# Performance work log

Hardware: AMD Instinct MI355X
Metric: run time of the kernel (lower is better)

## Reference

```python
import jax, jax.numpy as jnp
import numpy as np

N = 100000       # num nodes
E = 3200000      # num edges (avg degree 32)
F_IN = 128       # num_node_features
HID = 16         # hidden dim hard-coded in Net
C = 10           # num_classes


def setup_inputs() -> dict:
    key = jax.random.key(0)
    k1, k2, k3, k4 = jax.random.split(key, 4)
    x = jax.random.normal(k1, (N, F_IN), dtype=jnp.float32)
    edge_index = jax.random.randint(k2, (2, E), 0, N, dtype=jnp.int32)
    W1 = jax.random.normal(k3, (F_IN, HID), dtype=jnp.float32) * 0.05
    b1 = jnp.zeros((HID,), dtype=jnp.float32)
    W2 = jax.random.normal(k4, (HID, C), dtype=jnp.float32) * 0.05
    b2 = jnp.zeros((C,), dtype=jnp.float32)
    return {"x": x, "edge_index": edge_index, "W1": W1, "b1": b1, "W2": W2, "b2": b2}


def reference(x, edge_index, W1, b1, W2, b2):
    # GCNConv: out = D^{-1/2} (A + I) D^{-1/2} X W + b   (add self-loops)
    loops = jnp.arange(N, dtype=edge_index.dtype)
    row = jnp.concatenate([edge_index[0], loops])  # source nodes
    col = jnp.concatenate([edge_index[1], loops])  # target nodes

    # symmetric normalization (degrees include self-loops, so deg >= 1)
    deg = jax.ops.segment_sum(jnp.ones_like(col, dtype=jnp.float32), col, num_segments=N)
    dis = jax.lax.rsqrt(deg)
    norm = dis[row] * dis[col]  # [E+N]

    def gcn_conv(h, W, b):
        h = h @ W                               # [N, d_out] small GEMM first
        msg = h[row] * norm[:, None]            # gather + scale, [E+N, d_out]
        out = jax.ops.segment_sum(msg, col, num_segments=N)  # scatter-add
        return out + b

    h = jax.nn.relu(gcn_conv(x, W1, b1))
    # F.dropout(training=False) is identity in eval mode
    logits = gcn_conv(h, W2, b2)
    return jax.nn.log_softmax(logits, axis=1)
```

## Files before the change

### kernel.cpp

```cpp
#include <hip/hip_runtime.h>
#include <math.h>

#define N_NODES 100000
#define N_EDGES 3200000
#define F_IN 128
#define HID 16
#define C_OUT 10
#define WIN 256
#define NDIG 391
#define PNB2 500
#define EPB 6400
#define SCN (NDIG * PNB2)
#define SB1 764
#define MAXE2 20
#define CSRLDS 10240

typedef unsigned short u16;
typedef unsigned int u32;

__device__ __forceinline__ float bf2f(u16 u) {
    return __uint_as_float(((u32)u) << 16);
}
__device__ __forceinline__ u16 f2bf(float f) {
    u32 x = __float_as_uint(f);
    u32 r = (x + 0x7fffu + ((x >> 16) & 1u)) >> 16;
    return (u16)r;
}
__device__ __forceinline__ void acc8(float* a, uint4 w) {
    a[0] += bf2f((u16)(w.x & 0xffff)); a[1] += bf2f((u16)(w.x >> 16));
    a[2] += bf2f((u16)(w.y & 0xffff)); a[3] += bf2f((u16)(w.y >> 16));
    a[4] += bf2f((u16)(w.z & 0xffff)); a[5] += bf2f((u16)(w.z >> 16));
    a[6] += bf2f((u16)(w.w & 0xffff)); a[7] += bf2f((u16)(w.w >> 16));
}

__global__ void k_pcnt(const int* __restrict__ col, int* __restrict__ blkhistA) {
    __shared__ int h[NDIG];
    for (int i = threadIdx.x; i < NDIG; i += 256) h[i] = 0;
    __syncthreads();
    const uint4* c4 = (const uint4*)(col + blockIdx.x * EPB);
    for (int i = threadIdx.x; i < EPB / 4; i += 256) {
        uint4 c = c4[i];
        atomicAdd(&h[c.x >> 8], 1);
        atomicAdd(&h[c.y >> 8], 1);
        atomicAdd(&h[c.z >> 8], 1);
        atomicAdd(&h[c.w >> 8], 1);
    }
    __syncthreads();
    for (int d = threadIdx.x; d < NDIG; d += 256)
        blkhistA[d * PNB2 + blockIdx.x] = h[d];
}

__global__ void k_s1(const int* __restrict__ blkhistA, int* __restrict__ psum) {
    __shared__ int sm[256];
    int i = blockIdx.x * 256 + threadIdx.x;
    sm[threadIdx.x] = (i < SCN) ? blkhistA[i] : 0;
    __syncthreads();
    for (int off = 128; off > 0; off >>= 1) {
        if (threadIdx.x < off) sm[threadIdx.x] += sm[threadIdx.x + off];
        __syncthreads();
    }
    if (threadIdx.x == 0) psum[blockIdx.x] = sm[0];
}

__global__ void k_s3(const int* __restrict__ blkhistA, const int* __restrict__ psum,
                     int* __restrict__ blkhistB) {
    __shared__ int ps[1024];
    __shared__ int sm[256];
    int t = threadIdx.x;
    for (int i = t; i < 1024; i += 256) ps[i] = (i < SB1) ? psum[i] : 0;
    __syncthreads();
    for (int off = 1; off < 1024; off <<= 1) {
        int v[4];
#pragma unroll
        for (int j = 0; j < 4; j++) {
            int idx = t + j * 256;
            v[j] = ps[idx] + ((idx >= off) ? ps[idx - off] : 0);
        }
        __syncthreads();
#pragma unroll
        for (int j = 0; j < 4; j++) ps[t + j * 256] = v[j];
        __syncthreads();
    }
    int bpre = (blockIdx.x > 0) ? ps[blockIdx.x - 1] : 0;

    int i = blockIdx.x * 256 + t;
    int v = (i < SCN) ? blkhistA[i] : 0;
    sm[t] = v;
    __syncthreads();
    for (int off = 1; off < 256; off <<= 1) {
        int a = sm[t];
        int b = (t >= off) ? sm[t - off] : 0;
        __syncthreads();
        sm[t] = a + b;
        __syncthreads();
    }
    if (i < SCN) blkhistB[i] = bpre + sm[t] - v;
}

__global__ void __launch_bounds__(512) k_pwrite(
        const int* __restrict__ row, const int* __restrict__ col,
        const int* __restrict__ blkhistA, const int* __restrict__ blkhistB,
        u32* __restrict__ staging) {
    __shared__ u32 sorted[EPB];
    __shared__ u16 dwin[EPB];
    __shared__ int gbase[NDIG];
    __shared__ int lbase[NDIG];
    __shared__ int lcur[NDIG];
    __shared__ int scan[512];

    int t = threadIdx.x;
    int b = blockIdx.x;
    int hv = 0;
    if (t < NDIG) {
        hv = blkhistA[t * PNB2 + b];
        gbase[t] = blkhistB[t * PNB2 + b];
        lcur[t] = 0;
    }
    scan[t] = hv;
    __syncthreads();
    for (int off = 1; off < 512; off <<= 1) {
        int v = scan[t];
        int u = (t >= off) ? scan[t - off] : 0;
        __syncthreads();
        scan[t] = v + u;
        __syncthreads();
    }
    if (t < NDIG) lbase[t] = scan[t] - hv;
    __syncthreads();

    const uint4* c4 = (const uint4*)(col + b * EPB);
    const uint4* r4 = (const uint4*)(row + b * EPB);
    for (int i = t; i < EPB / 4; i += 512) {
        uint4 c = c4[i];
        uint4 r = r4[i];
        int d, rank, pos;
        d = (int)(c.x >> 8); rank = atomicAdd(&lcur[d], 1); pos = lbase[d] + rank;
        sorted[pos] = ((c.x & 255u) << 17) | r.x; dwin[pos] = (u16)d;
        d = (int)(c.y >> 8); rank = atomicAdd(&lcur[d], 1); pos = lbase[d] + rank;
        sorted[pos] = ((c.y & 255u) << 17) | r.y; dwin[pos] = (u16)d;
        d = (int)(c.z >> 8); rank = atomicAdd(&lcur[d], 1); pos = lbase[d] + rank;
        sorted[pos] = ((c.z & 255u) << 17) | r.z; dwin[pos] = (u16)d;
        d = (int)(c.w >> 8); rank = atomicAdd(&lcur[d], 1); pos = lbase[d] + rank;
        sorted[pos] = ((c.w & 255u) << 17) | r.w; dwin[pos] = (u16)d;
    }
    __syncthreads();

    for (int i = t; i < EPB; i += 512) {
        int d = dwin[i];
        staging[gbase[d] + (i - lbase[d])] = sorted[i];
    }
}

__global__ void __launch_bounds__(512) k_csr(
        u32* staging, const int* __restrict__ blkhistB,
        int* __restrict__ offs, float* __restrict__ dis) {
    __shared__ u32 sorted[CSRLDS];
    __shared__ int cnt[WIN];
    __shared__ int base[WIN];
    int w = blockIdx.x;
    int t = threadIdx.x;
    if (t < WIN) cnt[t] = 0;
    __syncthreads();
    int start = blkhistB[w * PNB2];
    int end = (w == NDIG - 1) ? N_EDGES : blkhistB[(w + 1) * PNB2];
    int m = end - start;
    u32 buf[MAXE2];
    int n = 0;
#pragma unroll
    for (int k = 0; k < MAXE2; k++) {
        int i = k * 512 + t;
        if (i < m) {
            u32 e = staging[start + i];
            buf[k] = e;
            n = k + 1;
            atomicAdd(&cnt[e >> 17], 1);
        }
    }
    __syncthreads();
    if (t < WIN) base[t] = cnt[t];
    __syncthreads();
    for (int off = 1; off < WIN; off <<= 1) {
        int v = 0;
        if (t < WIN) {
            v = base[t];
            if (t >= off) v += base[t - off];
        }
        __syncthreads();
        if (t < WIN) base[t] = v;
        __syncthreads();
    }
    if (t < WIN) {
        int excl = base[t] - cnt[t];
        base[t] = excl;
        int node = w * WIN + t;
        if (node < N_NODES) {
            offs[node] = start + excl;
            dis[node] = rsqrtf(1.0f + (float)cnt[t]);
        }
    }
    if (w == 0 && t == 0) offs[N_NODES] = N_EDGES;
    __syncthreads();
#pragma unroll
    for (int k = 0; k < MAXE2; k++) {
        if (k < n) {
            u32 e = buf[k];
            int pos = atomicAdd(&base[(int)(e >> 17)], 1);
            sorted[pos] = e;
        }
    }
    __syncthreads();
    for (int i = t; i < m; i += 512)
        staging[start + i] = sorted[i];
}

__global__ void k_gemm1(const float* __restrict__ x, const float* __restrict__ W1,
                        const float* __restrict__ dis, u16* __restrict__ h1s) {
    __shared__ float Ws[F_IN * HID];
    for (int t = threadIdx.x; t < F_IN * HID; t += blockDim.x) Ws[t] = W1[t];
    __syncthreads();

    int node = blockIdx.x * blockDim.x + threadIdx.x;
    if (node >= N_NODES) return;

    float acc[HID];
#pragma unroll
    for (int j = 0; j < HID; j++) acc[j] = 0.f;

    const float4* xr = (const float4*)(x + (size_t)node * F_IN);
#pragma unroll 2
    for (int k4 = 0; k4 < F_IN / 4; k4++) {
        float4 v = xr[k4];
        float xv[4] = {v.x, v.y, v.z, v.w};
#pragma unroll
        for (int kk = 0; kk < 4; kk++) {
            const float4* wr = (const float4*)(Ws + (k4 * 4 + kk) * HID);
            float4 w0 = wr[0], w1 = wr[1], w2 = wr[2], w3 = wr[3];
            float xs = xv[kk];
            acc[0]  += xs * w0.x; acc[1]  += xs * w0.y; acc[2]  += xs * w0.z; acc[3]  += xs * w0.w;
            acc[4]  += xs * w1.x; acc[5]  += xs * w1.y; acc[6]  += xs * w1.z; acc[7]  += xs * w1.w;
            acc[8]  += xs * w2.x; acc[9]  += xs * w2.y; acc[10] += xs * w2.z; acc[11] += xs * w2.w;
            acc[12] += xs * w3.x; acc[13] += xs * w3.y; acc[14] += xs * w3.z; acc[15] += xs * w3.w;
        }
    }

    float d = dis[node];
    u32 p[8];
#pragma unroll
    for (int i = 0; i < 8; i++)
        p[i] = (u32)f2bf(acc[2 * i] * d) | ((u32)f2bf(acc[2 * i + 1] * d) << 16);
    u32* dst = (u32*)(h1s + (size_t)node * HID);
#pragma unroll
    for (int i = 0; i < 8; i++) dst[i] = p[i];
}

__global__ void k_gl1(const int* __restrict__ offs, const u32* __restrict__ csr,
                      const float* __restrict__ dis, const u16* __restrict__ h1s,
                      const float* __restrict__ b1, const float* __restrict__ W2,
                      u16* __restrict__ h2s) {
    __shared__ float Ws[HID * C_OUT];
    __shared__ float b1s[HID];
    if (threadIdx.x < HID * C_OUT) Ws[threadIdx.x] = W2[threadIdx.x];
    if (threadIdx.x < HID) b1s[threadIdx.x] = b1[threadIdx.x];
    __syncthreads();

    int t = blockIdx.x * 256 + threadIdx.x;
    if (t >= N_NODES * 8) return;
    int node = t >> 3;
    int q = t & 7;
    int half = q >> 2;
    int eq = q & 3;
    const uint4* hb = (const uint4*)h1s;
    float a[8] = {0.f, 0.f, 0.f, 0.f, 0.f, 0.f, 0.f, 0.f};
    if (eq == 0) acc8(a, hb[(size_t)node * 2 + half]);
    int o = offs[node + half];
    int oo = __shfl_xor(o, 4);
    int s0 = half ? oo : o;
    int s1 = half ? o : oo;
    int len = s1 - s0;
    int lo = s0 + ((len * eq) >> 2);
    int hi = s0 + ((len * (eq + 1)) >> 2);
    int j = lo;
    for (; j < hi && (j & 3); j++)
        acc8(a, hb[(size_t)(csr[j] & 0x1FFFFu) * 2 + half]);
    for (; j + 4 <= hi; j += 4) {
        uint4 ss = *(const uint4*)(csr + j);
        uint4 w0 = hb[(size_t)(ss.x & 0x1FFFFu) * 2 + half];
        uint4 w1 = hb[(size_t)(ss.y & 0x1FFFFu) * 2 + half];
        uint4 w2 = hb[(size_t)(ss.z & 0x1FFFFu) * 2 + half];
        uint4 w3 = hb[(size_t)(ss.w & 0x1FFFFu) * 2 + half];
        acc8(a, w0); acc8(a, w1); acc8(a, w2); acc8(a, w3);
    }
    for (; j < hi; j++)
        acc8(a, hb[(size_t)(csr[j] & 0x1FFFFu) * 2 + half]);

#pragma unroll
    for (int k = 0; k < 8; k++) {
        a[k] += __shfl_xor(a[k], 1);
        a[k] += __shfl_xor(a[k], 2);
    }

    float dc = dis[node];
    float own[8], oth[8];
#pragma unroll
    for (int k = 0; k < 8; k++) own[k] = a[k] * dc;
#pragma unroll
    for (int k = 0; k < 8; k++) oth[k] = __shfl_xor(own[k], 4);
    float h[16];
#pragma unroll
    for (int k = 0; k < 8; k++) {
        h[k]     = half ? oth[k] : own[k];
        h[8 + k] = half ? own[k] : oth[k];
    }
#pragma unroll
    for (int jj = 0; jj < 16; jj++) h[jj] = fmaxf(h[jj] + b1s[jj], 0.f);

    int nf = half ? 2 : 8;
    float outv[8];
#pragma unroll
    for (int k = 0; k < 8; k++) {
        float s = 0.f;
        if (k < nf) {
            int kk = half * 8 + k;
#pragma unroll
            for (int jj = 0; jj < 16; jj++) s += h[jj] * Ws[jj * C_OUT + kk];
        }
        outv[k] = s * dc;
    }
    if (eq == 0) {
        uint4 ov;
        ov.x = (u32)f2bf(outv[0]) | ((u32)f2bf(outv[1]) << 16);
        ov.y = half ? 0u : ((u32)f2bf(outv[2]) | ((u32)f2bf(outv[3]) << 16));
        ov.z = half ? 0u : ((u32)f2bf(outv[4]) | ((u32)f2bf(outv[5]) << 16));
        ov.w = half ? 0u : ((u32)f2bf(outv[6]) | ((u32)f2bf(outv[7]) << 16));
        ((uint4*)h2s)[(size_t)node * 2 + half] = ov;
    }
}

__global__ void k_gather2(const int* __restrict__ offs, const u32* __restrict__ csr,
                          const float* __restrict__ dis, const u16* __restrict__ h2s,
                          const float* __restrict__ b2, float* __restrict__ out) {
    __shared__ float b2s[C_OUT];
    if (threadIdx.x < C_OUT) b2s[threadIdx.x] = b2[threadIdx.x];
    __syncthreads();

    int t = blockIdx.x * 256 + threadIdx.x;
    if (t >= N_NODES * 8) return;
    int node = t >> 3;
    int q = t & 7;
    int half = q >> 2;
    int eq = q & 3;
    const uint4* hb = (const uint4*)h2s;
    float a[8] = {0.f, 0.f, 0.f, 0.f, 0.f, 0.f, 0.f, 0.f};
    if (eq == 0) acc8(a, hb[(size_t)node * 2 + half]);
    int o = offs[node + half];
    int oo = __shfl_xor(o, 4);
    int s0 = half ? oo : o;
    int s1 = half ? o : oo;
    int len = s1 - s0;
    int lo = s0 + ((len * eq) >> 2);
    int hi = s0 + ((len * (eq + 1)) >> 2);
    int j = lo;
    for (; j < hi && (j & 3); j++)
        acc8(a, hb[(size_t)(csr[j] & 0x1FFFFu) * 2 + half]);
    for (; j + 4 <= hi; j += 4) {
        uint4 ss = *(const uint4*)(csr + j);
        uint4 w0 = hb[(size_t)(ss.x & 0x1FFFFu) * 2 + half];
        uint4 w1 = hb[(size_t)(ss.y & 0x1FFFFu) * 2 + half];
        uint4 w2 = hb[(size_t)(ss.z & 0x1FFFFu) * 2 + half];
        uint4 w3 = hb[(size_t)(ss.w & 0x1FFFFu) * 2 + half];
        acc8(a, w0); acc8(a, w1); acc8(a, w2); acc8(a, w3);
    }
    for (; j < hi; j++)
        acc8(a, hb[(size_t)(csr[j] & 0x1FFFFu) * 2 + half]);

#pragma unroll
    for (int k = 0; k < 8; k++) {
        a[k] += __shfl_xor(a[k], 1);
        a[k] += __shfl_xor(a[k], 2);
    }

    float dc = dis[node];
    int nf = half ? 2 : 8;
    float lg[8];
    float m = -1e30f;
#pragma unroll
    for (int k = 0; k < 8; k++) {
        lg[k] = a[k] * dc + b2s[(half * 8 + k) % C_OUT];
        if (k < nf) m = fmaxf(m, lg[k]);
    }
    m = fmaxf(m, __shfl_xor(m, 4));
    float s = 0.f;
#pragma unroll
    for (int k = 0; k < 8; k++)
        if (k < nf) s += expf(lg[k] - m);
    s += __shfl_xor(s, 4);
    float ls = logf(s) + m;
    if (eq == 0) {
        float* dst = out + (size_t)node * C_OUT + half * 8;
        if (half == 0) {
#pragma unroll
            for (int i = 0; i < 4; i++)
                *(float2*)(dst + 2 * i) = make_float2(lg[2 * i] - ls, lg[2 * i + 1] - ls);
        } else {
            *(float2*)dst = make_float2(lg[0] - ls, lg[1] - ls);
        }
    }
}

extern "C" void kernel_launch(void* const* d_in, const int* in_sizes, int n_in,
                              void* d_out, int out_size, void* d_ws, size_t ws_size,
                              hipStream_t stream) {
    const float* x  = (const float*)d_in[0];
    const int*   ei = (const int*)d_in[1];
    const float* W1 = (const float*)d_in[2];
    const float* b1 = (const float*)d_in[3];
    const float* W2 = (const float*)d_in[4];
    const float* b2 = (const float*)d_in[5];
    float* out = (float*)d_out;

    const int* row = ei;
    const int* col = ei + N_EDGES;

    char* ws = (char*)d_ws;
    float* dis      = (float*)(ws);
    int*   offs     = (int*)(ws + 400000);
    int*   blkhistA = (int*)(ws + 800016);
    int*   blkhistB = (int*)(ws + 1582352);
    int*   psum     = (int*)(ws + 2364688);
    u32*   staging  = (u32*)(ws + 2367744);
    u16*   h1s      = (u16*)(ws + 15167744);
    u16*   h2s      = (u16*)(ws + 18367744);

    const int B = 256;
    int gN  = (N_NODES + B - 1) / B;
    int gN8 = (N_NODES * 8 + B - 1) / B;

    k_pcnt  <<<PNB2, B, 0, stream>>>(col, blkhistA);
    k_s1    <<<SB1, B, 0, stream>>>(blkhistA, psum);
    k_s3    <<<SB1, B, 0, stream>>>(blkhistA, psum, blkhistB);
    k_pwrite<<<PNB2, 512, 0, stream>>>(row, col, blkhistA, blkhistB, staging);
    k_csr   <<<NDIG, 512, 0, stream>>>(staging, blkhistB, offs, dis);
    k_gemm1 <<<gN, B, 0, stream>>>(x, W1, dis, h1s);
    k_gl1   <<<gN8, B, 0, stream>>>(offs, staging, dis, h1s, b1, W2, h2s);
    k_gather2<<<gN8, B, 0, stream>>>(offs, staging, dis, h2s, b2, out);
}
```

Before: 212.2 us.

## Use nontemporal loads/stores for streaming data and unroll gather loops by eight

Replaces the streaming reads (edge indices, staging, x rows, CSR indices) and the final output stores with nontemporal builtins. This keeps single-use data from evicting the reused h1s/h2s rows from cache. It also adds an eight-wide unrolled gather loop in both aggregation kernels to keep more independent loads in flight. Launch bounds with a minimum of 8 blocks are added to constrain register use. The risks are higher register pressure from the unroll and little cache effect if the nontemporal hints do not change the load instructions the compiler emits.

```diff
diff --git a/kernel.cpp b/kernel.cpp
--- a/kernel.cpp
+++ b/kernel.cpp
@@ -17,6 +17,19 @@
 
 typedef unsigned short u16;
 typedef unsigned int u32;
+typedef u32 u32x4 __attribute__((ext_vector_type(4)));
+typedef float f32x4 __attribute__((ext_vector_type(4)));
+typedef float f32x2 __attribute__((ext_vector_type(2)));
+
+__device__ __forceinline__ u32x4 ntload4(const u32* p) {
+    return __builtin_nontemporal_load((const u32x4*)p);
+}
+__device__ __forceinline__ u32 ntload1(const u32* p) {
+    return __builtin_nontemporal_load(p);
+}
+__device__ __forceinline__ f32x4 ntloadf4(const float* p) {
+    return __builtin_nontemporal_load((const f32x4*)p);
+}
 
 __device__ __forceinline__ float bf2f(u16 u) {
     return __uint_as_float(((u32)u) << 16);
@@ -33,13 +46,13 @@
     a[6] += bf2f((u16)(w.w & 0xffff)); a[7] += bf2f((u16)(w.w >> 16));
 }
 
-__global__ void k_pcnt(const int* __restrict__ col, int* __restrict__ blkhistA) {
+__global__ void k_pcnt(const u32* __restrict__ col, int* __restrict__ blkhistA) {
     __shared__ int h[NDIG];
     for (int i = threadIdx.x; i < NDIG; i += 256) h[i] = 0;
     __syncthreads();
-    const uint4* c4 = (const uint4*)(col + blockIdx.x * EPB);
+    const u32* c4 = col + blockIdx.x * EPB;
     for (int i = threadIdx.x; i < EPB / 4; i += 256) {
-        uint4 c = c4[i];
+        u32x4 c = ntload4(c4 + i * 4);
         atomicAdd(&h[c.x >> 8], 1);
         atomicAdd(&h[c.y >> 8], 1);
         atomicAdd(&h[c.z >> 8], 1);
@@ -98,7 +111,7 @@
 }
 
 __global__ void __launch_bounds__(512) k_pwrite(
-        const int* __restrict__ row, const int* __restrict__ col,
+        const u32* __restrict__ row, const u32* __restrict__ col,
         const int* __restrict__ blkhistA, const int* __restrict__ blkhistB,
         u32* __restrict__ staging) {
     __shared__ u32 sorted[EPB];
@@ -128,11 +141,11 @@
     if (t < NDIG) lbase[t] = scan[t] - hv;
     __syncthreads();
 
-    const uint4* c4 = (const uint4*)(col + b * EPB);
-    const uint4* r4 = (const uint4*)(row + b * EPB);
+    const u32* c4 = col + b * EPB;
+    const u32* r4 = row + b * EPB;
     for (int i = t; i < EPB / 4; i += 512) {
-        uint4 c = c4[i];
-        uint4 r = r4[i];
+        u32x4 c = ntload4(c4 + i * 4);
+        u32x4 r = ntload4(r4 + i * 4);
         int d, rank, pos;
         d = (int)(c.x >> 8); rank = atomicAdd(&lcur[d], 1); pos = lbase[d] + rank;
         sorted[pos] = ((c.x & 255u) << 17) | r.x; dwin[pos] = (u16)d;
@@ -170,7 +183,7 @@
     for (int k = 0; k < MAXE2; k++) {
         int i = k * 512 + t;
         if (i < m) {
-            u32 e = staging[start + i];
+            u32 e = ntload1(staging + start + i);
             buf[k] = e;
             n = k + 1;
             atomicAdd(&cnt[e >> 17], 1);
@@ -226,10 +239,10 @@
 #pragma unroll
     for (int j = 0; j < HID; j++) acc[j] = 0.f;
 
-    const float4* xr = (const float4*)(x + (size_t)node * F_IN);
+    const float* xr = x + (size_t)node * F_IN;
 #pragma unroll 2
     for (int k4 = 0; k4 < F_IN / 4; k4++) {
-        float4 v = xr[k4];
+        f32x4 v = ntloadf4(xr + k4 * 4);
         float xv[4] = {v.x, v.y, v.z, v.w};
 #pragma unroll
         for (int kk = 0; kk < 4; kk++) {
@@ -253,10 +266,11 @@
     for (int i = 0; i < 8; i++) dst[i] = p[i];
 }
 
-__global__ void k_gl1(const int* __restrict__ offs, const u32* __restrict__ csr,
-                      const float* __restrict__ dis, const u16* __restrict__ h1s,
-                      const float* __restrict__ b1, const float* __restrict__ W2,
-                      u16* __restrict__ h2s) {
+__global__ void __launch_bounds__(256, 8) k_gl1(
+        const int* __restrict__ offs, const u32* __restrict__ csr,
+        const float* __restrict__ dis, const u16* __restrict__ h1s,
+        const float* __restrict__ b1, const float* __restrict__ W2,
+        u16* __restrict__ h2s) {
     __shared__ float Ws[HID * C_OUT];
     __shared__ float b1s[HID];
     if (threadIdx.x < HID * C_OUT) Ws[threadIdx.x] = W2[threadIdx.x];
@@ -281,9 +295,23 @@
     int hi = s0 + ((len * (eq + 1)) >> 2);
     int j = lo;
     for (; j < hi && (j & 3); j++)
-        acc8(a, hb[(size_t)(csr[j] & 0x1FFFFu) * 2 + half]);
+        acc8(a, hb[(size_t)(ntload1(csr + j) & 0x1FFFFu) * 2 + half]);
+    for (; j + 8 <= hi; j += 8) {
+        u32x4 sa = ntload4(csr + j);
+        u32x4 sb = ntload4(csr + j + 4);
+        uint4 w0 = hb[(size_t)(sa.x & 0x1FFFFu) * 2 + half];
+        uint4 w1 = hb[(size_t)(sa.y & 0x1FFFFu) * 2 + half];
+        uint4 w2 = hb[(size_t)(sa.z & 0x1FFFFu) * 2 + half];
+        uint4 w3 = hb[(size_t)(sa.w & 0x1FFFFu) * 2 + half];
+        uint4 w4 = hb[(size_t)(sb.x & 0x1FFFFu) * 2 + half];
+        uint4 w5 = hb[(size_t)(sb.y & 0x1FFFFu) * 2 + half];
+        uint4 w6 = hb[(size_t)(sb.z & 0x1FFFFu) * 2 + half];
+        uint4 w7 = hb[(size_t)(sb.w & 0x1FFFFu) * 2 + half];
+        acc8(a, w0); acc8(a, w1); acc8(a, w2); acc8(a, w3);
+        acc8(a, w4); acc8(a, w5); acc8(a, w6); acc8(a, w7);
+    }
     for (; j + 4 <= hi; j += 4) {
-        uint4 ss = *(const uint4*)(csr + j);
+        u32x4 ss = ntload4(csr + j);
         uint4 w0 = hb[(size_t)(ss.x & 0x1FFFFu) * 2 + half];
         uint4 w1 = hb[(size_t)(ss.y & 0x1FFFFu) * 2 + half];
         uint4 w2 = hb[(size_t)(ss.z & 0x1FFFFu) * 2 + half];
@@ -291,7 +319,7 @@
         acc8(a, w0); acc8(a, w1); acc8(a, w2); acc8(a, w3);
     }
     for (; j < hi; j++)
-        acc8(a, hb[(size_t)(csr[j] & 0x1FFFFu) * 2 + half]);
+        acc8(a, hb[(size_t)(ntload1(csr + j) & 0x1FFFFu) * 2 + half]);
 
 #pragma unroll
     for (int k = 0; k < 8; k++) {
@@ -336,9 +364,10 @@
     }
 }
 
-__global__ void k_gather2(const int* __restrict__ offs, const u32* __restrict__ csr,
-                          const float* __restrict__ dis, const u16* __restrict__ h2s,
-                          const float* __restrict__ b2, float* __restrict__ out) {
+__global__ void __launch_bounds__(256, 8) k_gather2(
+        const int* __restrict__ offs, const u32* __restrict__ csr,
+        const float* __restrict__ dis, const u16* __restrict__ h2s,
+        const float* __restrict__ b2, float* __restrict__ out) {
     __shared__ float b2s[C_OUT];
     if (threadIdx.x < C_OUT) b2s[threadIdx.x] = b2[threadIdx.x];
     __syncthreads();
@@ -361,9 +390,23 @@
     int hi = s0 + ((len * (eq + 1)) >> 2);
     int j = lo;
     for (; j < hi && (j & 3); j++)
-        acc8(a, hb[(size_t)(csr[j] & 0x1FFFFu) * 2 + half]);
+        acc8(a, hb[(size_t)(ntload1(csr + j) & 0x1FFFFu) * 2 + half]);
+    for (; j + 8 <= hi; j += 8) {
+        u32x4 sa = ntload4(csr + j);
+        u32x4 sb = ntload4(csr + j + 4);
+        uint4 w0 = hb[(size_t)(sa.x & 0x1FFFFu) * 2 + half];
+        uint4 w1 = hb[(size_t)(sa.y & 0x1FFFFu) * 2 + half];
+        uint4 w2 = hb[(size_t)(sa.z & 0x1FFFFu) * 2 + half];
+        uint4 w3 = hb[(size_t)(sa.w & 0x1FFFFu) * 2 + half];
+        uint4 w4 = hb[(size_t)(sb.x & 0x1FFFFu) * 2 + half];
+        uint4 w5 = hb[(size_t)(sb.y & 0x1FFFFu) * 2 + half];
+        uint4 w6 = hb[(size_t)(sb.z & 0x1FFFFu) * 2 + half];
+        uint4 w7 = hb[(size_t)(sb.w & 0x1FFFFu) * 2 + half];
+        acc8(a, w0); acc8(a, w1); acc8(a, w2); acc8(a, w3);
+        acc8(a, w4); acc8(a, w5); acc8(a, w6); acc8(a, w7);
+    }
     for (; j + 4 <= hi; j += 4) {
-        uint4 ss = *(const uint4*)(csr + j);
+        u32x4 ss = ntload4(csr + j);
         uint4 w0 = hb[(size_t)(ss.x & 0x1FFFFu) * 2 + half];
         uint4 w1 = hb[(size_t)(ss.y & 0x1FFFFu) * 2 + half];
         uint4 w2 = hb[(size_t)(ss.z & 0x1FFFFu) * 2 + half];
@@ -371,7 +414,7 @@
         acc8(a, w0); acc8(a, w1); acc8(a, w2); acc8(a, w3);
     }
     for (; j < hi; j++)
-        acc8(a, hb[(size_t)(csr[j] & 0x1FFFFu) * 2 + half]);
+        acc8(a, hb[(size_t)(ntload1(csr + j) & 0x1FFFFu) * 2 + half]);
 
 #pragma unroll
     for (int k = 0; k < 8; k++) {
@@ -399,10 +442,13 @@
         float* dst = out + (size_t)node * C_OUT + half * 8;
         if (half == 0) {
 #pragma unroll
-            for (int i = 0; i < 4; i++)
-                *(float2*)(dst + 2 * i) = make_float2(lg[2 * i] - ls, lg[2 * i + 1] - ls);
+            for (int i = 0; i < 4; i++) {
+                f32x2 v2 = {lg[2 * i] - ls, lg[2 * i + 1] - ls};
+                __builtin_nontemporal_store(v2, (f32x2*)(dst + 2 * i));
+            }
         } else {
-            *(float2*)dst = make_float2(lg[0] - ls, lg[1] - ls);
+            f32x2 v2 = {lg[0] - ls, lg[1] - ls};
+            __builtin_nontemporal_store(v2, (f32x2*)dst);
         }
     }
 }
@@ -418,8 +464,8 @@
     const float* b2 = (const float*)d_in[5];
     float* out = (float*)d_out;
 
-    const int* row = ei;
-    const int* col = ei + N_EDGES;
+    const u32* row = (const u32*)ei;
+    const u32* col = (const u32*)(ei + N_EDGES);
 
     char* ws = (char*)d_ws;
     float* dis      = (float*)(ws);
```

Result: slower. 306.3 us (+44.4%).
